# Kernel optimization log

Measured on AMD Instinct MI355X. Metric: run time of the kernel, lower is better.

## Reference

```python
import jax, jax.numpy as jnp
import numpy as np

N_USERS, N_ITEMS = 100000, 100000
N_NODES = N_USERS + N_ITEMS
N_EDGES = 4000000
USER_DIM, ITEM_DIM = 256, 128
COMMON, HIDDEN, OUT = 64, 64, 32


def setup_inputs() -> dict:
    key = jax.random.key(0)
    ks = jax.random.split(key, 12)
    inp = {
        "user_tensor": jax.random.normal(ks[0], (N_USERS, USER_DIM), jnp.float32),
        "item_tensor": jax.random.normal(ks[1], (N_ITEMS, ITEM_DIM), jnp.float32),
        "edge_index": jax.random.randint(ks[2], (2, N_EDGES), 0, N_NODES, jnp.int64),
        "edge_weight": jax.random.uniform(ks[3], (N_EDGES,), jnp.float32),
        # user_proj / item_proj (nn.Linear: y = x @ W + b)
        "Wu": jax.random.normal(ks[4], (USER_DIM, COMMON), jnp.float32) / np.sqrt(USER_DIM),
        "bu": jnp.zeros((COMMON,), jnp.float32),
        "Wi": jax.random.normal(ks[5], (ITEM_DIM, COMMON), jnp.float32) / np.sqrt(ITEM_DIM),
        "bi": jnp.zeros((COMMON,), jnp.float32),
        # GCNConv layers (linear without bias + separate bias)
        "W1": jax.random.normal(ks[6], (COMMON, HIDDEN), jnp.float32) / np.sqrt(COMMON),
        "b1": jnp.zeros((HIDDEN,), jnp.float32),
        "W2": jax.random.normal(ks[7], (HIDDEN, OUT), jnp.float32) / np.sqrt(HIDDEN),
        "b2": jnp.zeros((OUT,), jnp.float32),
    }
    return inp


def gcn_conv(x, W, b, src, dst, ew, num_nodes):
    """PyG GCNConv: add self-loops (weight 1), symmetric deg norm, transform, scatter-add."""
    x = x @ W  # transform first: [N, out]
    loop = jnp.arange(num_nodes, dtype=src.dtype)
    src2 = jnp.concatenate([src, loop])
    dst2 = jnp.concatenate([dst, loop])
    ew2 = jnp.concatenate([ew, jnp.ones((num_nodes,), x.dtype)])
    deg = jax.ops.segment_sum(ew2, dst2, num_segments=num_nodes)
    dinv = jnp.where(deg > 0, jax.lax.rsqrt(deg), 0.0)
    norm = dinv[src2] * ew2 * dinv[dst2]  # [E+N]
    msgs = x[src2] * norm[:, None]  # gather + scale: [E+N, out]
    return jax.ops.segment_sum(msgs, dst2, num_segments=num_nodes) + b


def reference(user_tensor, item_tensor, edge_index, edge_weight,
              Wu, bu, Wi, bi, W1, b1, W2, b2):
    user_emb = user_tensor @ Wu + bu
    item_emb = item_tensor @ Wi + bi
    x = jnp.concatenate([user_emb, item_emb], axis=0)  # [N_NODES, COMMON]
    src, dst = edge_index[0], edge_index[1]
    x = gcn_conv(x, W1, b1, src, dst, edge_weight, N_NODES)
    x = jax.nn.relu(x)
    x = gcn_conv(x, W2, b2, src, dst, edge_weight, N_NODES)
    return x
```

## Files before the change

### kernel.cpp

```cpp
#include <hip/hip_runtime.h>
#include <hip/hip_bf16.h>

#define N_USERS_C 100000
#define N_ITEMS_C 100000
#define N_NODES_C 200000
#define USER_DIM_C 256
#define ITEM_DIM_C 128
#define COMMON_C 64
#define HIDDEN_C 64
#define OUT_DIM_C 32

#define BUCKET_BITS 8
#define BUCKET_NODES 256
#define NBKT ((N_NODES_C + BUCKET_NODES - 1) / BUCKET_NODES)
#define BKT_CAP 6144
#define BIN_GRID 256

typedef unsigned int uint32;
typedef __bf16 bf16x8 __attribute__((ext_vector_type(8)));
typedef float f32x4 __attribute__((ext_vector_type(4)));


__device__ __forceinline__ float bf2f(ushort u) { return __uint_as_float(((unsigned)u) << 16); }
__device__ __forceinline__ ushort f2bf(float f) {
    unsigned u = __float_as_uint(f);
    return (ushort)((u + 0x7FFFu + ((u >> 16) & 1u)) >> 16);
}
__device__ __forceinline__ void store4(float* p, float a, float b, float c, float d) {
    *(float4*)p = make_float4(a, b, c, d);
}
__device__ __forceinline__ void store4(ushort* p, float a, float b, float c, float d) {
    ushort4 u;
    u.x = f2bf(a); u.y = f2bf(b); u.z = f2bf(c); u.w = f2bf(d);
    *(ushort4*)p = u;
}

union ABFrag {
    uint4 q;
    ushort u[8];
    bf16x8 v;
};


__global__ __launch_bounds__(1024) void bin_kernel(const int* __restrict__ src,
                                                   const int* __restrict__ dst,
                                                   const float* __restrict__ ew,
                                                   int* __restrict__ bucket_cnt,
                                                   int2* __restrict__ rec, int E, int chunk) {
    __shared__ int hist[NBKT];
    __shared__ int cur[NBKT];
    for (int i = threadIdx.x; i < NBKT; i += 1024) hist[i] = 0;
    __syncthreads();
    const int beg = blockIdx.x * chunk;
    const int end = min(E, beg + chunk);
    for (int e = beg + threadIdx.x; e < end; e += 1024)
        atomicAdd(&hist[dst[e] >> BUCKET_BITS], 1);
    __syncthreads();
    for (int i = threadIdx.x; i < NBKT; i += 1024)
        cur[i] = hist[i] ? atomicAdd(&bucket_cnt[i], hist[i]) : 0;
    __syncthreads();
    for (int e = beg + threadIdx.x; e < end; e += 1024) {
        int d = dst[e];
        uint32 q = (uint32)(ew[e] * 16383.0f + 0.5f);
        if (q > 16383u) q = 16383u;
        int b = d >> BUCKET_BITS;
        int slot = atomicAdd(&cur[b], 1);
        if (slot < BKT_CAP)
            rec[(size_t)b * BKT_CAP + slot] = make_int2((int)((((uint32)src[e]) << 14) | q), d);
    }
}


__global__ void bucket_build_kernel(const int2* __restrict__ rec,
                                    const int* __restrict__ bucket_cnt,
                                    uint32* __restrict__ csr, int* __restrict__ row_beg,
                                    int* __restrict__ row_cnt, float* __restrict__ dinv) {
    __shared__ int cnt[BUCKET_NODES];
    __shared__ float deg[BUCKET_NODES];
    __shared__ int s[BUCKET_NODES];
    __shared__ int cur[BUCKET_NODES];
    const int b = blockIdx.x;
    const int node0 = b << BUCKET_BITS;
    int total = bucket_cnt[b];
    if (total > BKT_CAP) total = BKT_CAP;
    const int2* r = rec + (size_t)b * BKT_CAP;
    cnt[threadIdx.x] = 0;
    deg[threadIdx.x] = 0.0f;
    __syncthreads();
    for (int j = threadIdx.x; j < total; j += 256) {
        int2 e = r[j];
        int dl = e.y - node0;
        atomicAdd(&cnt[dl], 1);
        atomicAdd(&deg[dl], (float)(((uint32)e.x) & 16383u) * (1.0f / 16383.0f));
    }
    __syncthreads();
    int v = cnt[threadIdx.x];
    s[threadIdx.x] = v;
    __syncthreads();
#pragma unroll
    for (int off = 1; off < 256; off <<= 1) {
        int t = (threadIdx.x >= off) ? s[threadIdx.x - off] : 0;
        __syncthreads();
        s[threadIdx.x] += t;
        __syncthreads();
    }
    const int ex = s[threadIdx.x] - v;
    const int node = node0 + threadIdx.x;
    const int abs0 = b * BKT_CAP + ex;
    if (node < N_NODES_C) {
        row_beg[node] = abs0;
        row_cnt[node] = v;
        dinv[node] = rsqrtf(1.0f + deg[threadIdx.x]);
    }
    cur[threadIdx.x] = abs0;
    __syncthreads();
    for (int j = threadIdx.x; j < total; j += 256) {
        int2 e = r[j];
        int dl = e.y - node0;
        int slot = atomicAdd(&cur[dl], 1);
        csr[slot] = (uint32)e.x;
    }
}


__device__ __forceinline__ void wt_one(const float* W, ushort* WT, int K, int N, int i) {
    int k = i / N, n = i % N;
    WT[(size_t)n * K + k] = f2bf(W[i]);
}

__global__ void wt_prep_kernel(const float* __restrict__ Wu, const float* __restrict__ Wi,
                               const float* __restrict__ W1, const float* __restrict__ W2,
                               ushort* __restrict__ wtU, ushort* __restrict__ wtI,
                               ushort* __restrict__ wt1, ushort* __restrict__ wt2) {
    const int SU = USER_DIM_C * 64, SI = ITEM_DIM_C * 64, S1 = 64 * 64, S2 = 64 * 32;
    int i = blockIdx.x * blockDim.x + threadIdx.x;
    if (i < SU) { wt_one(Wu, wtU, USER_DIM_C, 64, i); return; }
    i -= SU;
    if (i < SI) { wt_one(Wi, wtI, ITEM_DIM_C, 64, i); return; }
    i -= SI;
    if (i < S1) { wt_one(W1, wt1, 64, 64, i); return; }
    i -= S1;
    if (i < S2) wt_one(W2, wt2, 64, 32, i);
}

template <int K, int NT, bool XF32>
__global__ __launch_bounds__(256) void mfma_proj_kernel(const void* __restrict__ Xv,
                                                        const ushort* __restrict__ WT,
                                                        const float* __restrict__ bias,
                                                        ushort* __restrict__ Y, int M) {
    const int lane = threadIdx.x & 63;
    const int wave = threadIdx.x >> 6;
    const int lr = lane & 15;
    const int quad = lane >> 4;
    const int m0 = blockIdx.x * 64 + wave * 16;
    const int N = NT * 16;

    f32x4 acc[NT];
#pragma unroll
    for (int nt = 0; nt < NT; ++nt) acc[nt] = (f32x4){0.0f, 0.0f, 0.0f, 0.0f};

    int arow = m0 + lr;
    if (arow >= M) arow = M - 1;
    const size_t abase = (size_t)arow * K;

    for (int kc = 0; kc < K; kc += 32) {
        const int k0 = kc + quad * 8;
        ABFrag a;
        if (XF32) {
            const float* Xf = (const float*)Xv;
            float4 x0 = *(const float4*)(Xf + abase + k0);
            float4 x1 = *(const float4*)(Xf + abase + k0 + 4);
            a.u[0] = f2bf(x0.x); a.u[1] = f2bf(x0.y); a.u[2] = f2bf(x0.z); a.u[3] = f2bf(x0.w);
            a.u[4] = f2bf(x1.x); a.u[5] = f2bf(x1.y); a.u[6] = f2bf(x1.z); a.u[7] = f2bf(x1.w);
        } else {
            const ushort* Xb = (const ushort*)Xv;
            a.q = *(const uint4*)(Xb + abase + k0);
        }
#pragma unroll
        for (int nt = 0; nt < NT; ++nt) {
            ABFrag bf;
            bf.q = *(const uint4*)(WT + (size_t)(nt * 16 + lr) * K + k0);
            acc[nt] = __builtin_amdgcn_mfma_f32_16x16x32_bf16(a.v, bf.v, acc[nt], 0, 0, 0);
        }
    }

#pragma unroll
    for (int nt = 0; nt < NT; ++nt) {
        const int n = nt * 16 + lr;
        const float bc = bias ? bias[n] : 0.0f;
#pragma unroll
        for (int r = 0; r < 4; ++r) {
            int m = m0 + quad * 4 + r;
            if (m < M) Y[(size_t)m * N + n] = f2bf(acc[nt][r] + bc);
        }
    }
}

template <int N, bool RELU, typename TY>
__global__ void gather_kernel(const int* __restrict__ row_beg, const int* __restrict__ row_cnt,
                              const uint32* __restrict__ csr, const ushort* __restrict__ y,
                              const float* __restrict__ dinv, const float* __restrict__ b,
                              TY* __restrict__ out) {
    constexpr int LPN = N / 4;
    const int node = blockIdx.x * (256 / LPN) + threadIdx.x / LPN;
    const int c0 = (threadIdx.x % LPN) * 4;

    const int beg = row_beg[node];
    const int end = beg + row_cnt[node];

    float a0[4] = {0, 0, 0, 0}, a1[4] = {0, 0, 0, 0}, a2[4] = {0, 0, 0, 0}, a3[4] = {0, 0, 0, 0};
    int j = beg;
    for (; j + 4 <= end; j += 4) {
        uint32 e0 = csr[j], e1 = csr[j + 1], e2 = csr[j + 2], e3 = csr[j + 3];
        int s0 = e0 >> 14, s1 = e1 >> 14, s2 = e2 >> 14, s3 = e3 >> 14;
        float c0v = dinv[s0] * (float)(e0 & 16383u) * (1.0f / 16383.0f);
        float c1v = dinv[s1] * (float)(e1 & 16383u) * (1.0f / 16383.0f);
        float c2v = dinv[s2] * (float)(e2 & 16383u) * (1.0f / 16383.0f);
        float c3v = dinv[s3] * (float)(e3 & 16383u) * (1.0f / 16383.0f);
        ushort4 u0 = *(const ushort4*)(y + (size_t)s0 * N + c0);
        ushort4 u1 = *(const ushort4*)(y + (size_t)s1 * N + c0);
        ushort4 u2 = *(const ushort4*)(y + (size_t)s2 * N + c0);
        ushort4 u3 = *(const ushort4*)(y + (size_t)s3 * N + c0);
        a0[0] += bf2f(u0.x) * c0v; a0[1] += bf2f(u0.y) * c0v;
        a0[2] += bf2f(u0.z) * c0v; a0[3] += bf2f(u0.w) * c0v;
        a1[0] += bf2f(u1.x) * c1v; a1[1] += bf2f(u1.y) * c1v;
        a1[2] += bf2f(u1.z) * c1v; a1[3] += bf2f(u1.w) * c1v;
        a2[0] += bf2f(u2.x) * c2v; a2[1] += bf2f(u2.y) * c2v;
        a2[2] += bf2f(u2.z) * c2v; a2[3] += bf2f(u2.w) * c2v;
        a3[0] += bf2f(u3.x) * c3v; a3[1] += bf2f(u3.y) * c3v;
        a3[2] += bf2f(u3.z) * c3v; a3[3] += bf2f(u3.w) * c3v;
    }
    for (; j < end; ++j) {
        uint32 e = csr[j];
        int s = e >> 14;
        float cv = dinv[s] * (float)(e & 16383u) * (1.0f / 16383.0f);
        ushort4 u = *(const ushort4*)(y + (size_t)s * N + c0);
        a0[0] += bf2f(u.x) * cv; a0[1] += bf2f(u.y) * cv;
        a0[2] += bf2f(u.z) * cv; a0[3] += bf2f(u.w) * cv;
    }
    const float di = dinv[node];
    const float di2 = di * di;
    ushort4 us = *(const ushort4*)(y + (size_t)node * N + c0);
    float4 bc = *(const float4*)(b + c0);
    float r0 = ((a0[0] + a1[0]) + (a2[0] + a3[0])) * di + bf2f(us.x) * di2 + bc.x;
    float r1 = ((a0[1] + a1[1]) + (a2[1] + a3[1])) * di + bf2f(us.y) * di2 + bc.y;
    float r2 = ((a0[2] + a1[2]) + (a2[2] + a3[2])) * di + bf2f(us.z) * di2 + bc.z;
    float r3 = ((a0[3] + a1[3]) + (a2[3] + a3[3])) * di + bf2f(us.w) * di2 + bc.w;
    if (RELU) {
        r0 = fmaxf(r0, 0.0f); r1 = fmaxf(r1, 0.0f);
        r2 = fmaxf(r2, 0.0f); r3 = fmaxf(r3, 0.0f);
    }
    store4(&out[(size_t)node * N + c0], r0, r1, r2, r3);
}


extern "C" void kernel_launch(void* const* d_in, const int* in_sizes, int n_in,
                              void* d_out, int out_size, void* d_ws, size_t ws_size,
                              hipStream_t stream) {
    const float* user = (const float*)d_in[0];
    const float* item = (const float*)d_in[1];
    const int* ei = (const int*)d_in[2];
    const float* ew = (const float*)d_in[3];
    const float* Wu = (const float*)d_in[4];
    const float* bu = (const float*)d_in[5];
    const float* Wi = (const float*)d_in[6];
    const float* bi = (const float*)d_in[7];
    const float* W1 = (const float*)d_in[8];
    const float* b1 = (const float*)d_in[9];
    const float* W2 = (const float*)d_in[10];
    const float* b2 = (const float*)d_in[11];
    float* out = (float*)d_out;

    const int E = in_sizes[3];
    const int* src = ei;
    const int* dst = ei + E;
    const int NB = N_NODES_C;
    const int chunk = (E + BIN_GRID - 1) / BIN_GRID;

    char* p = (char*)d_ws;
    int2* rec = (int2*)p;      p += (size_t)NBKT * BKT_CAP * 8;
    uint32* csr = (uint32*)p;  p += (size_t)NBKT * BKT_CAP * 4;
    ushort* emb = (ushort*)p;  p += (size_t)NB * 64 * 2;
    ushort* y1 = (ushort*)p;   p += (size_t)NB * 64 * 2;
    ushort* h1 = (ushort*)p;   p += (size_t)NB * 64 * 2;
    ushort* y2 = (ushort*)p;   p += (size_t)NB * 32 * 2;
    int* bucket_cnt = (int*)p; p += (size_t)NBKT * 4;
    int* row_beg = (int*)p;    p += (size_t)NB * 4;
    int* row_cnt = (int*)p;    p += (size_t)NB * 4;
    float* dinv = (float*)p;   p += (size_t)NB * 4;
    ushort* wtU = (ushort*)p;  p += (size_t)USER_DIM_C * 64 * 2;
    ushort* wtI = (ushort*)p;  p += (size_t)ITEM_DIM_C * 64 * 2;
    ushort* wt1 = (ushort*)p;  p += (size_t)64 * 64 * 2;
    ushort* wt2 = (ushort*)p;  p += (size_t)64 * 32 * 2;

    hipMemsetAsync(bucket_cnt, 0, (size_t)NBKT * 4, stream);
    bin_kernel<<<BIN_GRID, 1024, 0, stream>>>(src, dst, ew, bucket_cnt, rec, E, chunk);
    bucket_build_kernel<<<NBKT, 256, 0, stream>>>(rec, bucket_cnt, csr, row_beg, row_cnt, dinv);

    wt_prep_kernel<<<120, 256, 0, stream>>>(Wu, Wi, W1, W2, wtU, wtI, wt1, wt2);

    mfma_proj_kernel<USER_DIM_C, 4, true><<<(N_USERS_C + 63) / 64, 256, 0, stream>>>(
        user, wtU, bu, emb, N_USERS_C);
    mfma_proj_kernel<ITEM_DIM_C, 4, true><<<(N_ITEMS_C + 63) / 64, 256, 0, stream>>>(
        item, wtI, bi, emb + (size_t)N_USERS_C * 64, N_ITEMS_C);

    mfma_proj_kernel<64, 4, false><<<NB / 64, 256, 0, stream>>>(emb, wt1, (const float*)nullptr,
                                                                y1, NB);
    gather_kernel<64, true><<<NB / 16, 256, 0, stream>>>(row_beg, row_cnt, csr, y1, dinv, b1, h1);

    mfma_proj_kernel<64, 2, false><<<NB / 64, 256, 0, stream>>>(h1, wt2, (const float*)nullptr,
                                                                y2, NB);
    gather_kernel<32, false><<<NB / 32, 256, 0, stream>>>(row_beg, row_cnt, csr, y2, dinv, b2, out);
}
```

Measured before the change: 582.8 us.

## Pack edge records to 32-bit, shrink buckets, prescale projections by dinv

Measured after the change: 558.8 us. 4.1% less time.

```diff
diff --git a/kernel.cpp b/kernel.cpp
--- a/kernel.cpp
+++ b/kernel.cpp
@@ -10,15 +10,16 @@
 #define HIDDEN_C 64
 #define OUT_DIM_C 32
 
-#define BUCKET_BITS 8
-#define BUCKET_NODES 256
-#define NBKT ((N_NODES_C + BUCKET_NODES - 1) / BUCKET_NODES)
-#define BKT_CAP 6144
+#define BUCKET_BITS 6
+#define BUCKET_NODES 64
+#define NBKT (N_NODES_C / BUCKET_NODES)
+#define BKT_CAP 1536
 #define BIN_GRID 256
 
 typedef unsigned int uint32;
 typedef __bf16 bf16x8 __attribute__((ext_vector_type(8)));
 typedef float f32x4 __attribute__((ext_vector_type(4)));
+
 
 
 __device__ __forceinline__ float bf2f(ushort u) { return __uint_as_float(((unsigned)u) << 16); }
@@ -46,7 +47,7 @@
                                                    const int* __restrict__ dst,
                                                    const float* __restrict__ ew,
                                                    int* __restrict__ bucket_cnt,
-                                                   int2* __restrict__ rec, int E, int chunk) {
+                                                   uint32* __restrict__ rec, int E, int chunk) {
     __shared__ int hist[NBKT];
     __shared__ int cur[NBKT];
     for (int i = threadIdx.x; i < NBKT; i += 1024) hist[i] = 0;
@@ -61,64 +62,63 @@
     __syncthreads();
     for (int e = beg + threadIdx.x; e < end; e += 1024) {
         int d = dst[e];
-        uint32 q = (uint32)(ew[e] * 16383.0f + 0.5f);
-        if (q > 16383u) q = 16383u;
+        uint32 q = (uint32)(ew[e] * 255.0f + 0.5f);
+        if (q > 255u) q = 255u;
         int b = d >> BUCKET_BITS;
         int slot = atomicAdd(&cur[b], 1);
         if (slot < BKT_CAP)
-            rec[(size_t)b * BKT_CAP + slot] = make_int2((int)((((uint32)src[e]) << 14) | q), d);
-    }
-}
-
-
-__global__ void bucket_build_kernel(const int2* __restrict__ rec,
+            rec[(size_t)b * BKT_CAP + slot] =
+                (((uint32)src[e]) << 14) | (q << 6) | (uint32)(d & (BUCKET_NODES - 1));
+    }
+}
+
+
+__global__ void bucket_build_kernel(const uint32* __restrict__ rec,
                                     const int* __restrict__ bucket_cnt,
                                     uint32* __restrict__ csr, int* __restrict__ row_beg,
                                     int* __restrict__ row_cnt, float* __restrict__ dinv) {
-    __shared__ int cnt[BUCKET_NODES];
-    __shared__ float deg[BUCKET_NODES];
+    __shared__ int pk[BUCKET_NODES];
     __shared__ int s[BUCKET_NODES];
     __shared__ int cur[BUCKET_NODES];
     const int b = blockIdx.x;
     const int node0 = b << BUCKET_BITS;
     int total = bucket_cnt[b];
     if (total > BKT_CAP) total = BKT_CAP;
-    const int2* r = rec + (size_t)b * BKT_CAP;
-    cnt[threadIdx.x] = 0;
-    deg[threadIdx.x] = 0.0f;
+    const uint32* r = rec + (size_t)b * BKT_CAP;
+    if (threadIdx.x < BUCKET_NODES) pk[threadIdx.x] = 0;
     __syncthreads();
     for (int j = threadIdx.x; j < total; j += 256) {
-        int2 e = r[j];
-        int dl = e.y - node0;
-        atomicAdd(&cnt[dl], 1);
-        atomicAdd(&deg[dl], (float)(((uint32)e.x) & 16383u) * (1.0f / 16383.0f));
-    }
-    __syncthreads();
-    int v = cnt[threadIdx.x];
-    s[threadIdx.x] = v;
-    __syncthreads();
-#pragma unroll
-    for (int off = 1; off < 256; off <<= 1) {
-        int t = (threadIdx.x >= off) ? s[threadIdx.x - off] : 0;
+        uint32 e = r[j];
+        atomicAdd(&pk[e & (BUCKET_NODES - 1)], (int)((1u << 20) | ((e >> 6) & 255u)));
+    }
+    __syncthreads();
+    int v = 0;
+    if (threadIdx.x < BUCKET_NODES) {
+        v = pk[threadIdx.x] >> 20;
+        s[threadIdx.x] = v;
+    }
+    __syncthreads();
+#pragma unroll
+    for (int off = 1; off < BUCKET_NODES; off <<= 1) {
+        int t = (threadIdx.x < BUCKET_NODES && threadIdx.x >= off) ? s[threadIdx.x - off] : 0;
         __syncthreads();
-        s[threadIdx.x] += t;
+        if (threadIdx.x < BUCKET_NODES) s[threadIdx.x] += t;
         __syncthreads();
     }
-    const int ex = s[threadIdx.x] - v;
-    const int node = node0 + threadIdx.x;
-    const int abs0 = b * BKT_CAP + ex;
-    if (node < N_NODES_C) {
+    if (threadIdx.x < BUCKET_NODES) {
+        const int ex = s[threadIdx.x] - v;
+        const int node = node0 + threadIdx.x;
+        const int abs0 = b * BKT_CAP + ex;
         row_beg[node] = abs0;
         row_cnt[node] = v;
-        dinv[node] = rsqrtf(1.0f + deg[threadIdx.x]);
-    }
-    cur[threadIdx.x] = abs0;
+        dinv[node] = rsqrtf(1.0f + (float)(pk[threadIdx.x] & 0xFFFFF) * (1.0f / 255.0f));
+        cur[threadIdx.x] = abs0;
+    }
     __syncthreads();
     for (int j = threadIdx.x; j < total; j += 256) {
-        int2 e = r[j];
-        int dl = e.y - node0;
-        int slot = atomicAdd(&cur[dl], 1);
-        csr[slot] = (uint32)e.x;
+        uint32 e = r[j];
+        int slot = atomicAdd(&cur[e & (BUCKET_NODES - 1)], 1);
+        csr[slot] = e;
     }
 }
 
@@ -143,10 +143,11 @@
     if (i < S2) wt_one(W2, wt2, 64, 32, i);
 }
 
-template <int K, int NT, bool XF32>
+template <int K, int NT, bool XF32, bool SCALE>
 __global__ __launch_bounds__(256) void mfma_proj_kernel(const void* __restrict__ Xv,
                                                         const ushort* __restrict__ WT,
                                                         const float* __restrict__ bias,
+                                                        const float* __restrict__ dinvp,
                                                         ushort* __restrict__ Y, int M) {
     const int lane = threadIdx.x & 63;
     const int wave = threadIdx.x >> 6;
@@ -185,13 +186,16 @@
     }
 
 #pragma unroll
-    for (int nt = 0; nt < NT; ++nt) {
-        const int n = nt * 16 + lr;
-        const float bc = bias ? bias[n] : 0.0f;
-#pragma unroll
-        for (int r = 0; r < 4; ++r) {
-            int m = m0 + quad * 4 + r;
-            if (m < M) Y[(size_t)m * N + n] = f2bf(acc[nt][r] + bc);
+    for (int r = 0; r < 4; ++r) {
+        const int m = m0 + quad * 4 + r;
+        if (m < M) {
+            const float sc = SCALE ? dinvp[m] : 1.0f;
+#pragma unroll
+            for (int nt = 0; nt < NT; ++nt) {
+                const int n = nt * 16 + lr;
+                const float bc = bias ? bias[n] : 0.0f;
+                Y[(size_t)m * N + n] = f2bf((acc[nt][r] + bc) * sc);
+            }
         }
     }
 }
@@ -213,10 +217,10 @@
     for (; j + 4 <= end; j += 4) {
         uint32 e0 = csr[j], e1 = csr[j + 1], e2 = csr[j + 2], e3 = csr[j + 3];
         int s0 = e0 >> 14, s1 = e1 >> 14, s2 = e2 >> 14, s3 = e3 >> 14;
-        float c0v = dinv[s0] * (float)(e0 & 16383u) * (1.0f / 16383.0f);
-        float c1v = dinv[s1] * (float)(e1 & 16383u) * (1.0f / 16383.0f);
-        float c2v = dinv[s2] * (float)(e2 & 16383u) * (1.0f / 16383.0f);
-        float c3v = dinv[s3] * (float)(e3 & 16383u) * (1.0f / 16383.0f);
+        float c0v = (float)((e0 >> 6) & 255u) * (1.0f / 255.0f);
+        float c1v = (float)((e1 >> 6) & 255u) * (1.0f / 255.0f);
+        float c2v = (float)((e2 >> 6) & 255u) * (1.0f / 255.0f);
+        float c3v = (float)((e3 >> 6) & 255u) * (1.0f / 255.0f);
         ushort4 u0 = *(const ushort4*)(y + (size_t)s0 * N + c0);
         ushort4 u1 = *(const ushort4*)(y + (size_t)s1 * N + c0);
         ushort4 u2 = *(const ushort4*)(y + (size_t)s2 * N + c0);
@@ -233,19 +237,18 @@
     for (; j < end; ++j) {
         uint32 e = csr[j];
         int s = e >> 14;
-        float cv = dinv[s] * (float)(e & 16383u) * (1.0f / 16383.0f);
+        float cv = (float)((e >> 6) & 255u) * (1.0f / 255.0f);
         ushort4 u = *(const ushort4*)(y + (size_t)s * N + c0);
         a0[0] += bf2f(u.x) * cv; a0[1] += bf2f(u.y) * cv;
         a0[2] += bf2f(u.z) * cv; a0[3] += bf2f(u.w) * cv;
     }
     const float di = dinv[node];
-    const float di2 = di * di;
     ushort4 us = *(const ushort4*)(y + (size_t)node * N + c0);
     float4 bc = *(const float4*)(b + c0);
-    float r0 = ((a0[0] + a1[0]) + (a2[0] + a3[0])) * di + bf2f(us.x) * di2 + bc.x;
-    float r1 = ((a0[1] + a1[1]) + (a2[1] + a3[1])) * di + bf2f(us.y) * di2 + bc.y;
-    float r2 = ((a0[2] + a1[2]) + (a2[2] + a3[2])) * di + bf2f(us.z) * di2 + bc.z;
-    float r3 = ((a0[3] + a1[3]) + (a2[3] + a3[3])) * di + bf2f(us.w) * di2 + bc.w;
+    float r0 = (((a0[0] + a1[0]) + (a2[0] + a3[0])) + bf2f(us.x)) * di + bc.x;
+    float r1 = (((a0[1] + a1[1]) + (a2[1] + a3[1])) + bf2f(us.y)) * di + bc.y;
+    float r2 = (((a0[2] + a1[2]) + (a2[2] + a3[2])) + bf2f(us.z)) * di + bc.z;
+    float r3 = (((a0[3] + a1[3]) + (a2[3] + a3[3])) + bf2f(us.w)) * di + bc.w;
     if (RELU) {
         r0 = fmaxf(r0, 0.0f); r1 = fmaxf(r1, 0.0f);
         r2 = fmaxf(r2, 0.0f); r3 = fmaxf(r3, 0.0f);
@@ -278,7 +281,7 @@
     const int chunk = (E + BIN_GRID - 1) / BIN_GRID;
 
     char* p = (char*)d_ws;
-    int2* rec = (int2*)p;      p += (size_t)NBKT * BKT_CAP * 8;
+    uint32* rec = (uint32*)p;  p += (size_t)NBKT * BKT_CAP * 4;
     uint32* csr = (uint32*)p;  p += (size_t)NBKT * BKT_CAP * 4;
     ushort* emb = (ushort*)p;  p += (size_t)NB * 64 * 2;
     ushort* y1 = (ushort*)p;   p += (size_t)NB * 64 * 2;
@@ -299,16 +302,16 @@
 
     wt_prep_kernel<<<120, 256, 0, stream>>>(Wu, Wi, W1, W2, wtU, wtI, wt1, wt2);
 
-    mfma_proj_kernel<USER_DIM_C, 4, true><<<(N_USERS_C + 63) / 64, 256, 0, stream>>>(
-        user, wtU, bu, emb, N_USERS_C);
-    mfma_proj_kernel<ITEM_DIM_C, 4, true><<<(N_ITEMS_C + 63) / 64, 256, 0, stream>>>(
-        item, wtI, bi, emb + (size_t)N_USERS_C * 64, N_ITEMS_C);
-
-    mfma_proj_kernel<64, 4, false><<<NB / 64, 256, 0, stream>>>(emb, wt1, (const float*)nullptr,
-                                                                y1, NB);
+    mfma_proj_kernel<USER_DIM_C, 4, true, false><<<(N_USERS_C + 63) / 64, 256, 0, stream>>>(
+        user, wtU, bu, nullptr, emb, N_USERS_C);
+    mfma_proj_kernel<ITEM_DIM_C, 4, true, false><<<(N_ITEMS_C + 63) / 64, 256, 0, stream>>>(
+        item, wtI, bi, nullptr, emb + (size_t)N_USERS_C * 64, N_ITEMS_C);
+
+    mfma_proj_kernel<64, 4, false, true><<<NB / 64, 256, 0, stream>>>(
+        emb, wt1, (const float*)nullptr, dinv, y1, NB);
     gather_kernel<64, true><<<NB / 16, 256, 0, stream>>>(row_beg, row_cnt, csr, y1, dinv, b1, h1);
 
-    mfma_proj_kernel<64, 2, false><<<NB / 64, 256, 0, stream>>>(h1, wt2, (const float*)nullptr,
-                                                                y2, NB);
+    mfma_proj_kernel<64, 2, false, true><<<NB / 64, 256, 0, stream>>>(
+        h1, wt2, (const float*)nullptr, dinv, y2, NB);
     gather_kernel<32, false><<<NB / 32, 256, 0, stream>>>(row_beg, row_cnt, csr, y2, dinv, b2, out);
 }
```
